# Performance work log

Measured on AMD Instinct MI355X. Metric: run time of the kernel, lower is better.

Reference implementation:

```python
import jax, jax.numpy as jnp
import numpy as np

B, N, L = 1, 128, 256
D_MSA, D_HID, D_PAIR = 256, 32, 128
EPS = 1e-5


def setup_inputs() -> dict:
    key = jax.random.key(0)
    ks = jax.random.split(key, 8)
    msa = jax.random.normal(ks[0], (B, N, L, D_MSA), dtype=jnp.float32)
    pair = jax.random.normal(ks[1], (B, L, L, D_PAIR), dtype=jnp.float32)
    symmids = jax.random.randint(ks[2], (1,), 0, 1, dtype=jnp.int64)
    symmsub = jax.random.randint(ks[3], (1,), 0, 1, dtype=jnp.int64)
    # learned params (lecun-normal-ish scale = 1/sqrt(fan_in))
    ln_gamma = jnp.ones((D_MSA,), jnp.float32)
    ln_beta = jnp.zeros((D_MSA,), jnp.float32)
    w_left = jax.random.normal(ks[4], (D_MSA, D_HID), jnp.float32) / np.sqrt(D_MSA)
    b_left = jnp.zeros((D_HID,), jnp.float32)
    w_right = jax.random.normal(ks[5], (D_MSA, D_HID), jnp.float32) / np.sqrt(D_MSA)
    b_right = jnp.zeros((D_HID,), jnp.float32)
    w_out = jax.random.normal(ks[6], (D_HID * D_HID, D_PAIR), jnp.float32) / np.sqrt(D_HID * D_HID)
    b_out = jnp.zeros((D_PAIR,), jnp.float32)
    return {
        "msa": msa, "pair": pair, "symmids": symmids, "symmsub": symmsub,
        "ln_gamma": ln_gamma, "ln_beta": ln_beta,
        "w_left": w_left, "b_left": b_left,
        "w_right": w_right, "b_right": b_right,
        "w_out": w_out, "b_out": b_out,
    }


def reference(msa, pair, symmids, symmsub, ln_gamma, ln_beta,
              w_left, b_left, w_right, b_right, w_out, b_out):
    b, n, l, _ = msa.shape
    # LayerNorm over d_msa (biased variance, matching torch)
    mu = jnp.mean(msa, axis=-1, keepdims=True)
    var = jnp.mean(jnp.square(msa - mu), axis=-1, keepdims=True)
    x = (msa - mu) * jax.lax.rsqrt(var + EPS) * ln_gamma + ln_beta
    left = x @ w_left + b_left                       # [b, n, l, d_h]
    right = (x @ w_right + b_right) / float(n)       # [b, n, l, d_h]
    # outer product, reduced over MSA (s) dim -> [b, l, m, d_h, d_h]
    out = jnp.einsum('bsli,bsmj->blmij', left, right).reshape(b, l, l, -1)
    out = out @ w_out + b_out                        # [b, l, l, d_pair]
    return pair + out
```

## Files before the change

kernel.cpp:

```cpp
#include <hip/hip_runtime.h>


typedef float v4f __attribute__((ext_vector_type(4)));
typedef short v8s __attribute__((ext_vector_type(8)));

static __device__ inline unsigned short f2bf(float x) {
    unsigned int u = __builtin_bit_cast(unsigned int, x);
    return (unsigned short)((u + 0x7fffu + ((u >> 16) & 1u)) >> 16);
}

__global__ __launch_bounds__(256) void k_prep(const float* __restrict__ w_out,
                                              const float* __restrict__ wl,
                                              const float* __restrict__ wr,
                                              unsigned short* __restrict__ w3,
                                              unsigned short* __restrict__ wTg) {
    const int b = blockIdx.x, t = threadIdx.x;
    unsigned short tmp[8];
    if (b < 64) {
        int tgt = b * 2048 + t * 8;
        int lane6 = (tgt >> 3) & 63, quad = lane6 >> 4, l15 = lane6 & 15;
        int w = (tgt >> 9) & 3, tt = (tgt >> 11) & 1;
        int inner = (tgt >> 12) & 1, ck = tgt >> 13;
        int p = w * 32 + tt * 16 + l15;
        for (int e = 0; e < 8; ++e) {
            int kp = ck * 64 + inner * 32 + quad * 8 + e;
            int j1 = (kp >> 9) & 1, qd = (kp >> 7) & 3, lp = (kp >> 3) & 15;
            int i1 = (kp >> 2) & 1, r = kp & 3;
            int ii = i1 * 16 + qd * 4 + r, jj = j1 * 16 + lp;
            tmp[e] = f2bf(w_out[(ii * 32 + jj) * 128 + p]);
        }
        *(uint4*)&w3[tgt] = *(const uint4*)tmp;
    } else {
        int tgt = (b - 64) * 2048 + t * 8;
        int c = tgt >> 8, d0 = tgt & 255;
        const float* src = (c < 32) ? wl : wr;
        int cc = c & 31;
        for (int e = 0; e < 8; ++e) tmp[e] = f2bf(src[(d0 + e) * 32 + cc]);
        *(uint4*)&wTg[tgt] = *(const uint4*)tmp;
    }
}

__global__ __launch_bounds__(256) void k_lnproj(
    const float* __restrict__ msa, const float* __restrict__ gamma, const float* __restrict__ beta,
    const unsigned short* __restrict__ wTg, const float* __restrict__ bl, const float* __restrict__ br,
    unsigned short* __restrict__ leftT, unsigned short* __restrict__ rightT) {
    __shared__ unsigned short xb[32 * 264];
    __shared__ unsigned short wlds[64 * 264];
    __shared__ unsigned short outT[64 * 40];

    const int t = threadIdx.x, lane = t & 63, w = t >> 6;
    const int l = blockIdx.x, s0 = blockIdx.y * 32;
    const int quad = lane >> 4, l15 = lane & 15;

    for (int it = 0; it < 8; ++it) {
        int idx = it * 2048 + t * 8;
        *(uint4*)&wlds[(idx >> 8) * 264 + (idx & 255)] = *(const uint4*)&wTg[idx];
    }

    float4 g4 = *(const float4*)&gamma[lane * 4];
    float4 be4 = *(const float4*)&beta[lane * 4];
    float4 vr[8]; float s1[8], s2[8];
    for (int r = 0; r < 8; ++r) {
        const float* row = msa + (size_t)((s0 + w * 8 + r) * 256 + l) * 256;
        vr[r] = *(const float4*)&row[lane * 4];
    }
    for (int r = 0; r < 8; ++r) {
        float4 v = vr[r];
        s1[r] = v.x + v.y + v.z + v.w;
        s2[r] = v.x * v.x + v.y * v.y + v.z * v.z + v.w * v.w;
    }
    for (int o = 32; o > 0; o >>= 1)
        for (int r = 0; r < 8; ++r) { s1[r] += __shfl_xor(s1[r], o); s2[r] += __shfl_xor(s2[r], o); }
    for (int r = 0; r < 8; ++r) {
        float mu = s1[r] * (1.f / 256);
        float rs = rsqrtf(s2[r] * (1.f / 256) - mu * mu + 1e-5f);
        float4 v = vr[r];
        ushort4 xs;
        xs.x = f2bf((v.x - mu) * rs * g4.x + be4.x);
        xs.y = f2bf((v.y - mu) * rs * g4.y + be4.y);
        xs.z = f2bf((v.z - mu) * rs * g4.z + be4.z);
        xs.w = f2bf((v.w - mu) * rs * g4.w + be4.w);
        *(ushort4*)&xb[(w * 8 + r) * 264 + lane * 4] = xs;
    }
    __syncthreads();

    const int mt = w >> 1, ntb = (w & 1) * 2;
    v4f acc[2] = {};
    const int frow = (mt * 16 + l15) * 264;
    for (int ks = 0; ks < 8; ++ks) {
        int k = ks * 32 + quad * 8;
        v8s a = *(const v8s*)&xb[frow + k];
        v8s b0 = *(const v8s*)&wlds[(ntb * 16 + l15) * 264 + k];
        v8s b1 = *(const v8s*)&wlds[((ntb + 1) * 16 + l15) * 264 + k];
        acc[0] = __builtin_amdgcn_mfma_f32_16x16x32_bf16(a, b0, acc[0], 0, 0, 0);
        acc[1] = __builtin_amdgcn_mfma_f32_16x16x32_bf16(a, b1, acc[1], 0, 0, 0);
    }

    for (int tn = 0; tn < 2; ++tn) {
        int c = (ntb + tn) * 16 + l15;
        float bias = c < 32 ? bl[c] : br[c - 32];
        float scale = c < 32 ? 1.f : (1.f / 128);
        for (int r = 0; r < 4; ++r)
            outT[c * 40 + mt * 16 + quad * 4 + r] = f2bf((acc[tn][r] + bias) * scale);
    }
    __syncthreads();

    {
        int c = t >> 2, q = t & 3;
        uint4 vv = *(const uint4*)&outT[c * 40 + q * 8];
        int cc = c & 31;
        unsigned short* base = (c < 32) ? leftT : rightT;
        unsigned short* dst = base + l * 4096 + blockIdx.y * 1024
                            + (cc >> 4) * 512 + q * 128 + (cc & 15) * 8;
        *(uint4*)dst = vv;
    }
}

__global__ __launch_bounds__(256, 3) void k_outer(
    const unsigned short* __restrict__ leftT, const unsigned short* __restrict__ rightT,
    const unsigned short* __restrict__ w2g, const float* __restrict__ bout,
    const float* __restrict__ pairIn, float* __restrict__ out) {
    __shared__ alignas(16) unsigned short Obuf[16384];

    const int t = threadIdx.x, lane = t & 63, w = t >> 6;
    const int l0 = blockIdx.x * 4, m0 = blockIdx.y * 4;
    const int wm = w & 1, wn = w >> 1;
    const int quad = lane >> 4, l15 = lane & 15;

    float pf[8];
#pragma unroll
    for (int tt = 0; tt < 2; ++tt)
#pragma unroll
        for (int r = 0; r < 4; ++r) {
            int pr = quad * 4 + r;
            int dl = pr >> 2, dm = pr & 3;
            int p = (w * 2 + tt) * 16 + l15;
            size_t idx = (size_t)((l0 + dl) * 256 + (m0 + dm)) * 128 + p;
            pf[tt * 4 + r] = pairIn[idx];
        }

    const unsigned short* Asrc = leftT + l0 * 4096;
    const unsigned short* Bsrc = rightT + m0 * 4096;

    v4f acc[4][4] = {};
#pragma unroll
    for (int kk = 0; kk < 4; ++kk) {
        v8s a[4], bb[4];
#pragma unroll
        for (int i = 0; i < 4; ++i)
            a[i] = *(const v8s*)&Asrc[(wm * 2 + (i >> 1)) * 4096 + kk * 1024 + (i & 1) * 512 + lane * 8];
#pragma unroll
        for (int j = 0; j < 4; ++j)
            bb[j] = *(const v8s*)&Bsrc[(wn * 2 + (j >> 1)) * 4096 + kk * 1024 + (j & 1) * 512 + lane * 8];
#pragma unroll
        for (int i = 0; i < 4; ++i)
#pragma unroll
            for (int j = 0; j < 4; ++j)
                acc[i][j] = __builtin_amdgcn_mfma_f32_16x16x32_bf16(a[i], bb[j], acc[i][j], 0, 0, 0);
    }

    for (int a2 = 0; a2 < 2; ++a2)
        for (int b2 = 0; b2 < 2; ++b2) {
            int pr = (wm * 2 + a2) * 4 + wn * 2 + b2;
            for (int j1 = 0; j1 < 2; ++j1) {
                unsigned short tmp8[8];
                for (int i1 = 0; i1 < 2; ++i1)
                    for (int r = 0; r < 4; ++r)
                        tmp8[i1 * 4 + r] = f2bf(acc[a2 * 2 + i1][b2 * 2 + j1][r]);
                int pg = (j1 * 64 + lane) ^ (pr & 7) ^ ((pr & 8) << 3);
                *(uint4*)&Obuf[pr * 1024 + pg * 8] = *(const uint4*)tmp8;
            }
        }
    __syncthreads();

    v4f acc2[2] = {};
    {
        const unsigned short* wsrc = w2g + w * 512 + lane * 8;
        v8s f0 = *(const v8s*)&wsrc[0];
        v8s f1 = *(const v8s*)&wsrc[2048];
        v8s f2 = *(const v8s*)&wsrc[4096];
        v8s f3 = *(const v8s*)&wsrc[6144];
#pragma unroll
        for (int ck = 0; ck < 16; ++ck) {
            v8s c0 = f0, c1 = f1, c2 = f2, c3 = f3;
            if (ck < 15) {
                const unsigned short* nx = wsrc + (ck + 1) * 8192;
                f0 = *(const v8s*)&nx[0];
                f1 = *(const v8s*)&nx[2048];
                f2 = *(const v8s*)&nx[4096];
                f3 = *(const v8s*)&nx[6144];
            }
            {
                int g = ck * 8 + quad;
                v8s a = *(const v8s*)&Obuf[l15 * 1024 + ((g ^ (l15 & 7) ^ ((l15 & 8) << 3)) << 3)];
                acc2[0] = __builtin_amdgcn_mfma_f32_16x16x32_bf16(a, c0, acc2[0], 0, 0, 0);
                acc2[1] = __builtin_amdgcn_mfma_f32_16x16x32_bf16(a, c1, acc2[1], 0, 0, 0);
            }
            {
                int g = ck * 8 + 4 + quad;
                v8s a = *(const v8s*)&Obuf[l15 * 1024 + ((g ^ (l15 & 7) ^ ((l15 & 8) << 3)) << 3)];
                acc2[0] = __builtin_amdgcn_mfma_f32_16x16x32_bf16(a, c2, acc2[0], 0, 0, 0);
                acc2[1] = __builtin_amdgcn_mfma_f32_16x16x32_bf16(a, c3, acc2[1], 0, 0, 0);
            }
        }
    }

#pragma unroll
    for (int tt = 0; tt < 2; ++tt) {
        int p = (w * 2 + tt) * 16 + l15;
        float bo = bout[p];
#pragma unroll
        for (int r = 0; r < 4; ++r) {
            int pr = quad * 4 + r;
            int dl = pr >> 2, dm = pr & 3;
            size_t idx = (size_t)((l0 + dl) * 256 + (m0 + dm)) * 128 + p;
            out[idx] = pf[tt * 4 + r] + bo + acc2[tt][r];
        }
    }
}

extern "C" void kernel_launch(void* const* d_in, const int* in_sizes, int n_in,
                              void* d_out, int out_size, void* d_ws, size_t ws_size,
                              hipStream_t stream) {
    const float* msa   = (const float*)d_in[0];
    const float* pairI = (const float*)d_in[1];
    const float* gamma = (const float*)d_in[4];
    const float* beta  = (const float*)d_in[5];
    const float* wl    = (const float*)d_in[6];
    const float* bl    = (const float*)d_in[7];
    const float* wr    = (const float*)d_in[8];
    const float* br    = (const float*)d_in[9];
    const float* wout  = (const float*)d_in[10];
    const float* bout  = (const float*)d_in[11];
    float* out = (float*)d_out;

    unsigned short* leftT  = (unsigned short*)d_ws;
    unsigned short* rightT = leftT + 256 * 32 * 128;
    unsigned short* w3     = rightT + 256 * 32 * 128;
    unsigned short* wTg    = w3 + 131072;

    k_prep<<<dim3(72), 256, 0, stream>>>(wout, wl, wr, w3, wTg);
    k_lnproj<<<dim3(256, 4), 256, 0, stream>>>(msa, gamma, beta, wTg, bl, br, leftT, rightT);
    k_outer<<<dim3(64, 64), 256, 0, stream>>>(leftT, rightT, w3, bout, pairI, out);
}
```

Baseline: 185.2 us.

## Enlarge outer-product tile to 8x4 pairs with 512-thread blocks

Doubles the k_outer block tile from 4x4 to 8x4 (l,m) pairs and uses 8 waves per block. Each wave now covers 16 of the 128 output channels across 32 pairs instead of 32 channels across 16 pairs. This halves the per-block w_out fragment loads relative to work done. The cost is a doubled LDS buffer (64KB), a changed weight layout in k_prep, and possibly lower occupancy at 512 threads.

```diff
diff --git a/kernel.cpp b/kernel.cpp
--- a/kernel.cpp
+++ b/kernel.cpp
@@ -19,9 +19,9 @@
     if (b < 64) {
         int tgt = b * 2048 + t * 8;
         int lane6 = (tgt >> 3) & 63, quad = lane6 >> 4, l15 = lane6 & 15;
-        int w = (tgt >> 9) & 3, tt = (tgt >> 11) & 1;
+        int w = (tgt >> 9) & 7;
         int inner = (tgt >> 12) & 1, ck = tgt >> 13;
-        int p = w * 32 + tt * 16 + l15;
+        int p = w * 16 + l15;
         for (int e = 0; e < 8; ++e) {
             int kp = ck * 64 + inner * 32 + quad * 8 + e;
             int j1 = (kp >> 9) & 1, qd = (kp >> 7) & 3, lp = (kp >> 3) & 15;
@@ -116,27 +116,29 @@
     }
 }
 
-__global__ __launch_bounds__(256, 3) void k_outer(
+__global__ __launch_bounds__(512, 4) void k_outer(
     const unsigned short* __restrict__ leftT, const unsigned short* __restrict__ rightT,
     const unsigned short* __restrict__ w2g, const float* __restrict__ bout,
     const float* __restrict__ pairIn, float* __restrict__ out) {
-    __shared__ alignas(16) unsigned short Obuf[16384];
+    __shared__ alignas(16) unsigned short Obuf[32768];
 
     const int t = threadIdx.x, lane = t & 63, w = t >> 6;
-    const int l0 = blockIdx.x * 4, m0 = blockIdx.y * 4;
-    const int wm = w & 1, wn = w >> 1;
+    const int l0 = blockIdx.x * 8, m0 = blockIdx.y * 4;
+    const int wm = w & 3, wn = w >> 2;
     const int quad = lane >> 4, l15 = lane & 15;
 
-    float pf[8];
-#pragma unroll
-    for (int tt = 0; tt < 2; ++tt)
+    const unsigned short* wsrc = w2g + w * 512 + lane * 8;
+    v8s f0 = *(const v8s*)&wsrc[0];
+    v8s f1 = *(const v8s*)&wsrc[4096];
+    const int p = w * 16 + l15;
+    float pfv[8];
+#pragma unroll
+    for (int pm = 0; pm < 2; ++pm)
 #pragma unroll
         for (int r = 0; r < 4; ++r) {
-            int pr = quad * 4 + r;
-            int dl = pr >> 2, dm = pr & 3;
-            int p = (w * 2 + tt) * 16 + l15;
-            size_t idx = (size_t)((l0 + dl) * 256 + (m0 + dm)) * 128 + p;
-            pf[tt * 4 + r] = pairIn[idx];
+            int P = pm * 16 + quad * 4 + r;
+            size_t idx = (size_t)((l0 + (P >> 2)) * 256 + (m0 + (P & 3))) * 128 + p;
+            pfv[pm * 4 + r] = pairIn[idx];
         }
 
     const unsigned short* Asrc = leftT + l0 * 4096;
@@ -161,62 +163,54 @@
 
     for (int a2 = 0; a2 < 2; ++a2)
         for (int b2 = 0; b2 < 2; ++b2) {
-            int pr = (wm * 2 + a2) * 4 + wn * 2 + b2;
+            int P = (wm * 2 + a2) * 4 + wn * 2 + b2;
             for (int j1 = 0; j1 < 2; ++j1) {
                 unsigned short tmp8[8];
                 for (int i1 = 0; i1 < 2; ++i1)
                     for (int r = 0; r < 4; ++r)
                         tmp8[i1 * 4 + r] = f2bf(acc[a2 * 2 + i1][b2 * 2 + j1][r]);
-                int pg = (j1 * 64 + lane) ^ (pr & 7) ^ ((pr & 8) << 3);
-                *(uint4*)&Obuf[pr * 1024 + pg * 8] = *(const uint4*)tmp8;
+                int pg = (j1 * 64 + lane) ^ (P & 7) ^ ((P & 8) << 3);
+                *(uint4*)&Obuf[P * 1024 + pg * 8] = *(const uint4*)tmp8;
             }
         }
     __syncthreads();
 
     v4f acc2[2] = {};
-    {
-        const unsigned short* wsrc = w2g + w * 512 + lane * 8;
-        v8s f0 = *(const v8s*)&wsrc[0];
-        v8s f1 = *(const v8s*)&wsrc[2048];
-        v8s f2 = *(const v8s*)&wsrc[4096];
-        v8s f3 = *(const v8s*)&wsrc[6144];
-#pragma unroll
-        for (int ck = 0; ck < 16; ++ck) {
-            v8s c0 = f0, c1 = f1, c2 = f2, c3 = f3;
-            if (ck < 15) {
-                const unsigned short* nx = wsrc + (ck + 1) * 8192;
-                f0 = *(const v8s*)&nx[0];
-                f1 = *(const v8s*)&nx[2048];
-                f2 = *(const v8s*)&nx[4096];
-                f3 = *(const v8s*)&nx[6144];
-            }
-            {
-                int g = ck * 8 + quad;
-                v8s a = *(const v8s*)&Obuf[l15 * 1024 + ((g ^ (l15 & 7) ^ ((l15 & 8) << 3)) << 3)];
-                acc2[0] = __builtin_amdgcn_mfma_f32_16x16x32_bf16(a, c0, acc2[0], 0, 0, 0);
-                acc2[1] = __builtin_amdgcn_mfma_f32_16x16x32_bf16(a, c1, acc2[1], 0, 0, 0);
-            }
-            {
-                int g = ck * 8 + 4 + quad;
-                v8s a = *(const v8s*)&Obuf[l15 * 1024 + ((g ^ (l15 & 7) ^ ((l15 & 8) << 3)) << 3)];
-                acc2[0] = __builtin_amdgcn_mfma_f32_16x16x32_bf16(a, c2, acc2[0], 0, 0, 0);
-                acc2[1] = __builtin_amdgcn_mfma_f32_16x16x32_bf16(a, c3, acc2[1], 0, 0, 0);
-            }
-        }
-    }
-
-#pragma unroll
-    for (int tt = 0; tt < 2; ++tt) {
-        int p = (w * 2 + tt) * 16 + l15;
-        float bo = bout[p];
+#pragma unroll
+    for (int ck = 0; ck < 16; ++ck) {
+        v8s c0 = f0, c1 = f1;
+        if (ck < 15) {
+            const unsigned short* nx = wsrc + (ck + 1) * 8192;
+            f0 = *(const v8s*)&nx[0];
+            f1 = *(const v8s*)&nx[4096];
+        }
+        {
+            int g = ck * 8 + quad;
+            int ch = ((g ^ (l15 & 7) ^ ((l15 & 8) << 3)) << 3);
+            v8s a0 = *(const v8s*)&Obuf[l15 * 1024 + ch];
+            v8s a1 = *(const v8s*)&Obuf[(16 + l15) * 1024 + ch];
+            acc2[0] = __builtin_amdgcn_mfma_f32_16x16x32_bf16(a0, c0, acc2[0], 0, 0, 0);
+            acc2[1] = __builtin_amdgcn_mfma_f32_16x16x32_bf16(a1, c0, acc2[1], 0, 0, 0);
+        }
+        {
+            int g = ck * 8 + 4 + quad;
+            int ch = ((g ^ (l15 & 7) ^ ((l15 & 8) << 3)) << 3);
+            v8s a0 = *(const v8s*)&Obuf[l15 * 1024 + ch];
+            v8s a1 = *(const v8s*)&Obuf[(16 + l15) * 1024 + ch];
+            acc2[0] = __builtin_amdgcn_mfma_f32_16x16x32_bf16(a0, c1, acc2[0], 0, 0, 0);
+            acc2[1] = __builtin_amdgcn_mfma_f32_16x16x32_bf16(a1, c1, acc2[1], 0, 0, 0);
+        }
+    }
+
+    float bo = bout[p];
+#pragma unroll
+    for (int pm = 0; pm < 2; ++pm)
 #pragma unroll
         for (int r = 0; r < 4; ++r) {
-            int pr = quad * 4 + r;
-            int dl = pr >> 2, dm = pr & 3;
-            size_t idx = (size_t)((l0 + dl) * 256 + (m0 + dm)) * 128 + p;
-            out[idx] = pf[tt * 4 + r] + bo + acc2[tt][r];
-        }
-    }
+            int P = pm * 16 + quad * 4 + r;
+            size_t idx = (size_t)((l0 + (P >> 2)) * 256 + (m0 + (P & 3))) * 128 + p;
+            out[idx] = pfv[pm * 4 + r] + bo + acc2[pm][r];
+        }
 }
 
 extern "C" void kernel_launch(void* const* d_in, const int* in_sizes, int n_in,
@@ -241,5 +235,5 @@
 
     k_prep<<<dim3(72), 256, 0, stream>>>(wout, wl, wr, w3, wTg);
     k_lnproj<<<dim3(256, 4), 256, 0, stream>>>(msa, gamma, beta, wTg, bl, br, leftT, rightT);
-    k_outer<<<dim3(64, 64), 256, 0, stream>>>(leftT, rightT, w3, bout, pairI, out);
-}
+    k_outer<<<dim3(32, 64), 512, 0, stream>>>(leftT, rightT, w3, bout, pairI, out);
+}
```

New measurement: 209.5 us. +13.1%, slower.

## Stage outer-product operands through LDS via async global-to-LDS loads

Applied to the files above, without the earlier changes.

The first GEMM in k_outer now copies the left and right tiles into shared memory in two K halves using global_load_lds, then reads MFMA fragments from LDS instead of loading each fragment straight from global memory. The shared buffer is reused for the bf16 intermediate, and the first w_out fragments are prefetched before the store-out phase. The second GEMM splits its accumulation into two independent chains to shorten MFMA dependency stalls, and launch bounds rise to 4 blocks per SM. The changes aim to cut redundant global traffic and latency, at the cost of extra barriers and more register pressure under the tighter occupancy bound.

```diff
diff --git a/kernel.cpp b/kernel.cpp
--- a/kernel.cpp
+++ b/kernel.cpp
@@ -7,6 +7,13 @@
 static __device__ inline unsigned short f2bf(float x) {
     unsigned int u = __builtin_bit_cast(unsigned int, x);
     return (unsigned short)((u + 0x7fffu + ((u >> 16) & 1u)) >> 16);
+}
+
+static __device__ inline void gl_lds16(const unsigned short* g, unsigned short* l) {
+    __builtin_amdgcn_global_load_lds(
+        (const __attribute__((address_space(1))) unsigned int*)g,
+        (__attribute__((address_space(3))) unsigned int*)(unsigned long long)l,
+        16, 0, 0);
 }
 
 __global__ __launch_bounds__(256) void k_prep(const float* __restrict__ w_out,
@@ -116,11 +123,14 @@
     }
 }
 
-__global__ __launch_bounds__(256, 3) void k_outer(
+__global__ __launch_bounds__(256, 4) void k_outer(
     const unsigned short* __restrict__ leftT, const unsigned short* __restrict__ rightT,
     const unsigned short* __restrict__ w2g, const float* __restrict__ bout,
     const float* __restrict__ pairIn, float* __restrict__ out) {
-    __shared__ alignas(16) unsigned short Obuf[16384];
+    __shared__ alignas(16) unsigned short smem[16384];
+    unsigned short* Ah = smem;
+    unsigned short* Bh = smem + 8192;
+    unsigned short* Obuf = smem;
 
     const int t = threadIdx.x, lane = t & 63, w = t >> 6;
     const int l0 = blockIdx.x * 4, m0 = blockIdx.y * 4;
@@ -133,9 +143,8 @@
 #pragma unroll
         for (int r = 0; r < 4; ++r) {
             int pr = quad * 4 + r;
-            int dl = pr >> 2, dm = pr & 3;
             int p = (w * 2 + tt) * 16 + l15;
-            size_t idx = (size_t)((l0 + dl) * 256 + (m0 + dm)) * 128 + p;
+            size_t idx = (size_t)((l0 + (pr >> 2)) * 256 + (m0 + (pr & 3))) * 128 + p;
             pf[tt * 4 + r] = pairIn[idx];
         }
 
@@ -143,65 +152,75 @@
     const unsigned short* Bsrc = rightT + m0 * 4096;
 
     v4f acc[4][4] = {};
-#pragma unroll
-    for (int kk = 0; kk < 4; ++kk) {
-        v8s a[4], bb[4];
-#pragma unroll
-        for (int i = 0; i < 4; ++i)
-            a[i] = *(const v8s*)&Asrc[(wm * 2 + (i >> 1)) * 4096 + kk * 1024 + (i & 1) * 512 + lane * 8];
-#pragma unroll
-        for (int j = 0; j < 4; ++j)
-            bb[j] = *(const v8s*)&Bsrc[(wn * 2 + (j >> 1)) * 4096 + kk * 1024 + (j & 1) * 512 + lane * 8];
-#pragma unroll
-        for (int i = 0; i < 4; ++i)
+    for (int kh = 0; kh < 2; ++kh) {
+        if (kh) __syncthreads();
+#pragma unroll
+        for (int it = 0; it < 4; ++it) {
+            int x = (it * 256 + t) * 8;
+            gl_lds16(&Asrc[(x >> 11) * 4096 + kh * 2048 + (x & 2047)], &Ah[x]);
+            gl_lds16(&Bsrc[(x >> 11) * 4096 + kh * 2048 + (x & 2047)], &Bh[x]);
+        }
+        __syncthreads();
+#pragma unroll
+        for (int kl = 0; kl < 2; ++kl) {
+            v8s a[4], bb[4];
+#pragma unroll
+            for (int i = 0; i < 4; ++i)
+                a[i] = *(const v8s*)&Ah[(wm * 2 + (i >> 1)) * 2048 + kl * 1024 + (i & 1) * 512 + lane * 8];
 #pragma unroll
             for (int j = 0; j < 4; ++j)
-                acc[i][j] = __builtin_amdgcn_mfma_f32_16x16x32_bf16(a[i], bb[j], acc[i][j], 0, 0, 0);
-    }
+                bb[j] = *(const v8s*)&Bh[(wn * 2 + (j >> 1)) * 2048 + kl * 1024 + (j & 1) * 512 + lane * 8];
+#pragma unroll
+            for (int i = 0; i < 4; ++i)
+#pragma unroll
+                for (int j = 0; j < 4; ++j)
+                    acc[i][j] = __builtin_amdgcn_mfma_f32_16x16x32_bf16(a[i], bb[j], acc[i][j], 0, 0, 0);
+        }
+    }
+    __syncthreads();
+
+    const unsigned short* wsrc = w2g + w * 512 + lane * 8;
+    v8s f0 = *(const v8s*)&wsrc[0];
+    v8s f1 = *(const v8s*)&wsrc[2048];
+    v8s f2 = *(const v8s*)&wsrc[4096];
+    v8s f3 = *(const v8s*)&wsrc[6144];
 
     for (int a2 = 0; a2 < 2; ++a2)
         for (int b2 = 0; b2 < 2; ++b2) {
-            int pr = (wm * 2 + a2) * 4 + wn * 2 + b2;
+            int P = (wm * 2 + a2) * 4 + wn * 2 + b2;
             for (int j1 = 0; j1 < 2; ++j1) {
                 unsigned short tmp8[8];
                 for (int i1 = 0; i1 < 2; ++i1)
                     for (int r = 0; r < 4; ++r)
                         tmp8[i1 * 4 + r] = f2bf(acc[a2 * 2 + i1][b2 * 2 + j1][r]);
-                int pg = (j1 * 64 + lane) ^ (pr & 7) ^ ((pr & 8) << 3);
-                *(uint4*)&Obuf[pr * 1024 + pg * 8] = *(const uint4*)tmp8;
+                int pg = (j1 * 64 + lane) ^ (P & 7) ^ ((P & 8) << 3);
+                *(uint4*)&Obuf[P * 1024 + pg * 8] = *(const uint4*)tmp8;
             }
         }
     __syncthreads();
 
-    v4f acc2[2] = {};
-    {
-        const unsigned short* wsrc = w2g + w * 512 + lane * 8;
-        v8s f0 = *(const v8s*)&wsrc[0];
-        v8s f1 = *(const v8s*)&wsrc[2048];
-        v8s f2 = *(const v8s*)&wsrc[4096];
-        v8s f3 = *(const v8s*)&wsrc[6144];
-#pragma unroll
-        for (int ck = 0; ck < 16; ++ck) {
-            v8s c0 = f0, c1 = f1, c2 = f2, c3 = f3;
-            if (ck < 15) {
-                const unsigned short* nx = wsrc + (ck + 1) * 8192;
-                f0 = *(const v8s*)&nx[0];
-                f1 = *(const v8s*)&nx[2048];
-                f2 = *(const v8s*)&nx[4096];
-                f3 = *(const v8s*)&nx[6144];
-            }
-            {
-                int g = ck * 8 + quad;
-                v8s a = *(const v8s*)&Obuf[l15 * 1024 + ((g ^ (l15 & 7) ^ ((l15 & 8) << 3)) << 3)];
-                acc2[0] = __builtin_amdgcn_mfma_f32_16x16x32_bf16(a, c0, acc2[0], 0, 0, 0);
-                acc2[1] = __builtin_amdgcn_mfma_f32_16x16x32_bf16(a, c1, acc2[1], 0, 0, 0);
-            }
-            {
-                int g = ck * 8 + 4 + quad;
-                v8s a = *(const v8s*)&Obuf[l15 * 1024 + ((g ^ (l15 & 7) ^ ((l15 & 8) << 3)) << 3)];
-                acc2[0] = __builtin_amdgcn_mfma_f32_16x16x32_bf16(a, c2, acc2[0], 0, 0, 0);
-                acc2[1] = __builtin_amdgcn_mfma_f32_16x16x32_bf16(a, c3, acc2[1], 0, 0, 0);
-            }
+    v4f aI0[2] = {}, aI1[2] = {};
+#pragma unroll
+    for (int ck = 0; ck < 16; ++ck) {
+        v8s c0 = f0, c1 = f1, c2 = f2, c3 = f3;
+        if (ck < 15) {
+            const unsigned short* nx = wsrc + (ck + 1) * 8192;
+            f0 = *(const v8s*)&nx[0];
+            f1 = *(const v8s*)&nx[2048];
+            f2 = *(const v8s*)&nx[4096];
+            f3 = *(const v8s*)&nx[6144];
+        }
+        {
+            int g = ck * 8 + quad;
+            v8s a = *(const v8s*)&Obuf[l15 * 1024 + ((g ^ (l15 & 7) ^ ((l15 & 8) << 3)) << 3)];
+            aI0[0] = __builtin_amdgcn_mfma_f32_16x16x32_bf16(a, c0, aI0[0], 0, 0, 0);
+            aI0[1] = __builtin_amdgcn_mfma_f32_16x16x32_bf16(a, c1, aI0[1], 0, 0, 0);
+        }
+        {
+            int g = ck * 8 + 4 + quad;
+            v8s a = *(const v8s*)&Obuf[l15 * 1024 + ((g ^ (l15 & 7) ^ ((l15 & 8) << 3)) << 3)];
+            aI1[0] = __builtin_amdgcn_mfma_f32_16x16x32_bf16(a, c2, aI1[0], 0, 0, 0);
+            aI1[1] = __builtin_amdgcn_mfma_f32_16x16x32_bf16(a, c3, aI1[1], 0, 0, 0);
         }
     }
 
@@ -209,12 +228,12 @@
     for (int tt = 0; tt < 2; ++tt) {
         int p = (w * 2 + tt) * 16 + l15;
         float bo = bout[p];
+        v4f acc2 = aI0[tt] + aI1[tt];
 #pragma unroll
         for (int r = 0; r < 4; ++r) {
             int pr = quad * 4 + r;
-            int dl = pr >> 2, dm = pr & 3;
-            size_t idx = (size_t)((l0 + dl) * 256 + (m0 + dm)) * 128 + p;
-            out[idx] = pf[tt * 4 + r] + bo + acc2[tt][r];
+            size_t idx = (size_t)((l0 + (pr >> 2)) * 256 + (m0 + (pr & 3))) * 128 + p;
+            out[idx] = pf[tt * 4 + r] + bo + acc2[r];
         }
     }
 }
```

Result: faster. 180.1 us (-2.8%).
